# Kernel optimization log

Hardware: AMD Instinct MI355X
Metric: run time of the kernel (lower is better)

The kernel has to match this reference:

```python
import jax, jax.numpy as jnp
import numpy as np

B, N, F_IN, F_OUT, OUT = 32, 1024, 128, 128, 1


def setup_inputs() -> dict:
    key = jax.random.key(0)
    k = jax.random.split(key, 6)
    A = jax.random.uniform(k[0], (B, N, N), dtype=jnp.float32)
    H = jax.random.normal(k[1], (B, N, F_IN), dtype=jnp.float32)
    W = jax.random.normal(k[2], (F_IN, F_OUT), dtype=jnp.float32)
    b = jax.random.normal(k[3], (F_OUT,), dtype=jnp.float32)
    fc_w = jax.random.normal(k[4], (OUT, F_OUT), dtype=jnp.float32)
    fc_b = jax.random.normal(k[5], (OUT,), dtype=jnp.float32)
    return {"A": A, "H": H, "W": W, "b": b, "fc_w": fc_w, "fc_b": fc_b}


def reference(A, H, W, b, fc_w, fc_b):
    n = A.shape[1]
    A_tilde = A + jnp.eye(n, dtype=A.dtype)          # [B,N,N] add self-loops
    d = jnp.sum(A_tilde, axis=1)                      # [B,N] degrees (col sums, matches torch dim=1)
    inv_sqrt_d = 1.0 / jnp.sqrt(d)                    # elementwise, equivalent to sqrt(inv(diag(d)))
    # D^-1/2 A_tilde D^-1/2 as row/col scaling (avoids diag_embed + matrix inverse)
    A_norm = inv_sqrt_d[:, :, None] * A_tilde * inv_sqrt_d[:, None, :]
    h = jax.nn.relu(jnp.einsum('bij,bjf,fo->bio', A_norm, H, W) + b)  # GCN layer
    pooled = jnp.sum(h, axis=1)                       # [B,F_OUT] sum pooling over nodes
    return pooled @ fc_w.T + fc_b                     # [B,OUT]
```

## Files before the change

### kernel.cpp

```cpp
#include <hip/hip_runtime.h>
#include <hip/hip_bf16.h>

#define NB 32
#define NN 1024
#define FF 128

typedef __attribute__((ext_vector_type(8))) short short8;
typedef __attribute__((ext_vector_type(4))) float f32x4;

static __device__ __forceinline__ unsigned short f2bf(float x) {
  unsigned int u = __float_as_uint(x);
  u += 0x7fffu + ((u >> 16) & 1u);
  return (unsigned short)(u >> 16);
}

static __device__ __forceinline__ unsigned long long pack4bf(float a, float b, float c, float d) {
  return (unsigned long long)f2bf(a)
       | ((unsigned long long)f2bf(b) << 16)
       | ((unsigned long long)f2bf(c) << 32)
       | ((unsigned long long)f2bf(d) << 48);
}

static __device__ __forceinline__ void gl16(const void* g, void* l) {
  __builtin_amdgcn_global_load_lds((const __attribute__((address_space(1))) void*)g,
                                   (__attribute__((address_space(3))) void*)l, 16, 0, 0);
}

__global__ __launch_bounds__(256) void k1_colsum_cvt(const float* __restrict__ A,
                                                     unsigned short* __restrict__ Ab,
                                                     float* __restrict__ partial) {
  int t = threadIdx.x;
  int s = blockIdx.x;
  int b = blockIdx.y;
  const float* base = A + (size_t)b * NN * NN + (size_t)(s * 64) * NN + (t << 2);
  unsigned short* obase = Ab + (size_t)b * NN * NN + (size_t)(s * 64) * NN + (t << 2);
  int jj = t << 2;
  bool diag_band = ((t >> 4) == s);
  float4 sum = make_float4(0.f, 0.f, 0.f, 0.f);
  #pragma unroll 8
  for (int i = 0; i < 64; ++i) {
    float4 v = *reinterpret_cast<const float4*>(base + (size_t)i * NN);
    if (diag_band) {
      int gi = (s << 6) + i;
      v.x += (gi == jj)     ? 1.f : 0.f;
      v.y += (gi == jj + 1) ? 1.f : 0.f;
      v.z += (gi == jj + 2) ? 1.f : 0.f;
      v.w += (gi == jj + 3) ? 1.f : 0.f;
    }
    sum.x += v.x; sum.y += v.y; sum.z += v.z; sum.w += v.w;
    *reinterpret_cast<unsigned long long*>(obase + (size_t)i * NN) =
        pack4bf(v.x, v.y, v.z, v.w);
  }
  *reinterpret_cast<float4*>(partial + (((b << 4) + s) << 10) + jj) = sum;
}

__global__ void k2_finalize(const float* __restrict__ partial, const float* __restrict__ W,
                            float* __restrict__ isd, float* __restrict__ pooled,
                            unsigned short* __restrict__ Wt) {
  int idx = blockIdx.x * 256 + threadIdx.x;
  int b = idx >> 10, j = idx & 1023;
  float d = 0.0f;
  #pragma unroll
  for (int s = 0; s < 16; ++s) d += partial[(((b << 4) + s) << 10) + j];
  isd[idx] = rsqrtf(d);
  if (idx < 4096) pooled[idx] = 0.f;
  if (idx < 16384) {
    int o = idx >> 7, k = idx & 127;
    Wt[idx] = f2bf(W[k * FF + o]);
  }
}

__global__ __launch_bounds__(512) void k3_hw(const float* __restrict__ H,
                                             const unsigned short* __restrict__ Wt,
                                             const float* __restrict__ isd,
                                             unsigned short* __restrict__ HWpT) {
  __shared__ unsigned short Ws[128][136];
  __shared__ unsigned short Hs[128][136];
  int jblk = blockIdx.x;
  int b = blockIdx.y;
  int tid = threadIdx.x, wave = tid >> 6, lane = tid & 63;

  {
    int r = tid >> 4, c = (tid & 15) << 3;
    #pragma unroll
    for (int p = 0; p < 4; ++p) {
      int row = r + (p << 5);
      *reinterpret_cast<short8*>(&Ws[row][c]) =
          *reinterpret_cast<const short8*>(Wt + row * FF + c);
    }
  }
  {
    int r = tid >> 5, c = (tid & 31) << 2;
    const float* Hbase = H + (size_t)b * NN * FF + (size_t)(jblk * 128) * FF;
    #pragma unroll
    for (int p = 0; p < 8; ++p) {
      int row = r + (p << 4);
      const float4 v = *reinterpret_cast<const float4*>(Hbase + (size_t)row * FF + c);
      *reinterpret_cast<unsigned long long*>(&Hs[row][c]) = pack4bf(v.x, v.y, v.z, v.w);
    }
  }
  __syncthreads();

  f32x4 acc[8];
  #pragma unroll
  for (int i = 0; i < 8; ++i) acc[i] = (f32x4){0.f, 0.f, 0.f, 0.f};

  int mrow = (wave << 4) + (lane & 15);
  int koff = (lane >> 4) << 3;
  #pragma unroll
  for (int kk = 0; kk < 4; ++kk) {
    short8 af = *reinterpret_cast<const short8*>(&Ws[mrow][(kk << 5) + koff]);
    #pragma unroll
    for (int nf = 0; nf < 8; ++nf) {
      short8 bf = *reinterpret_cast<const short8*>(&Hs[(nf << 4) + (lane & 15)][(kk << 5) + koff]);
      acc[nf] = __builtin_amdgcn_mfma_f32_16x16x32_bf16(af, bf, acc[nf], 0, 0, 0);
    }
  }

  int fbase = (wave << 4) + ((lane >> 4) << 2);
  #pragma unroll
  for (int nf = 0; nf < 8; ++nf) {
    int j = (jblk << 7) + (nf << 4) + (lane & 15);
    float sc = isd[(b << 10) + j];
    size_t outb = (size_t)b * FF * NN + (size_t)j;
    #pragma unroll
    for (int r = 0; r < 4; ++r) {
      HWpT[outb + (size_t)(fbase + r) * NN] = f2bf(acc[nf][r] * sc);
    }
  }
}

__global__ __launch_bounds__(256) void k4_gcn(const unsigned short* __restrict__ Ab,
                                              const unsigned short* __restrict__ HWpT,
                                              const float* __restrict__ isd,
                                              const float* __restrict__ bias,
                                              float* __restrict__ pooled) {
  __shared__ unsigned short As[64 * 64];
  __shared__ unsigned short Bs[128 * 64];
  int iblk = blockIdx.x;
  int b = blockIdx.y;
  int tid = threadIdx.x, wave = tid >> 6, lane = tid & 63;
  int i0 = iblk * 64;

  f32x4 acc[8];
  #pragma unroll
  for (int i = 0; i < 8; ++i) acc[i] = (f32x4){0.f, 0.f, 0.f, 0.f};

  int schunk = (lane & 7) ^ (lane >> 3);
  int arow = (wave << 4) + (lane >> 3);
  int brow = (wave << 5) + (lane >> 3);
  const unsigned short* aSrc = Ab + (size_t)b * NN * NN + (size_t)(i0 + arow) * NN + (schunk << 3);
  const unsigned short* bSrc = HWpT + (size_t)b * FF * NN + (size_t)brow * NN + (schunk << 3);
  char* asBase = (char*)As + wave * 2048;
  char* bsBase = (char*)Bs + wave * 4096;

  int mrow = (wave << 4) + (lane & 15);
  int q16 = (lane >> 4) << 4;
  int aoff0 = (mrow * 128 + q16) ^ ((mrow & 7) << 4);

  for (int k0 = 0; k0 < NN; k0 += 64) {
    gl16(aSrc,               asBase);
    gl16(aSrc + 8 * NN,      asBase + 1024);
    gl16(bSrc,               bsBase);
    gl16(bSrc + 8 * NN,      bsBase + 1024);
    gl16(bSrc + 16 * NN,     bsBase + 2048);
    gl16(bSrc + 24 * NN,     bsBase + 3072);
    __syncthreads();
    #pragma unroll
    for (int kk = 0; kk < 2; ++kk) {
      const short8 af = *reinterpret_cast<const short8*>((const char*)As + (aoff0 ^ (kk << 6)));
      #pragma unroll
      for (int nf = 0; nf < 8; ++nf) {
        int br = (nf << 4) + (lane & 15);
        const short8 bf = *reinterpret_cast<const short8*>(
            (const char*)Bs + ((br * 128 + kk * 64 + q16) ^ ((br & 7) << 4)));
        acc[nf] = __builtin_amdgcn_mfma_f32_16x16x32_bf16(af, bf, acc[nf], 0, 0, 0);
      }
    }
    __syncthreads();
    aSrc += 64; bSrc += 64;
  }

  int irow = i0 + (wave << 4) + ((lane >> 4) << 2);
  float sc0 = isd[(b << 10) + irow];
  float sc1 = isd[(b << 10) + irow + 1];
  float sc2 = isd[(b << 10) + irow + 2];
  float sc3 = isd[(b << 10) + irow + 3];
  #pragma unroll
  for (int nf = 0; nf < 8; ++nf) {
    float bi = bias[(nf << 4) + (lane & 15)];
    float s = fmaxf(acc[nf][0] * sc0 + bi, 0.f)
            + fmaxf(acc[nf][1] * sc1 + bi, 0.f)
            + fmaxf(acc[nf][2] * sc2 + bi, 0.f)
            + fmaxf(acc[nf][3] * sc3 + bi, 0.f);
    s += __shfl_xor(s, 16);
    s += __shfl_xor(s, 32);
    if (lane < 16) atomicAdd(&pooled[(b << 7) + (nf << 4) + lane], s);
  }
}

__global__ void k5_out(const float* __restrict__ pooled, const float* __restrict__ fcw,
                       const float* __restrict__ fcb, float* __restrict__ out) {
  int b = blockIdx.x, t = threadIdx.x;
  float s = pooled[(b << 7) + t] * fcw[t] + pooled[(b << 7) + 64 + t] * fcw[64 + t];
  #pragma unroll
  for (int off = 1; off < 64; off <<= 1) s += __shfl_xor(s, off);
  if (t == 0) out[b] = s + fcb[0];
}

extern "C" void kernel_launch(void* const* d_in, const int* in_sizes, int n_in,
                              void* d_out, int out_size, void* d_ws, size_t ws_size,
                              hipStream_t stream) {
  const float* A    = (const float*)d_in[0];
  const float* H    = (const float*)d_in[1];
  const float* W    = (const float*)d_in[2];
  const float* bias = (const float*)d_in[3];
  const float* fcw  = (const float*)d_in[4];
  const float* fcb  = (const float*)d_in[5];
  float* out = (float*)d_out;

  float* ws = (float*)d_ws;
  float* partial = ws;
  float* isd     = ws + 524288;
  float* pooled  = ws + 524288 + 32768;
  unsigned short* Wt   = (unsigned short*)(ws + 524288 + 32768 + 4096);
  unsigned short* HWpT = Wt + 16384;
  unsigned short* Ab   = HWpT + (size_t)NB * FF * NN;

  k1_colsum_cvt<<<dim3(16, 32), 256, 0, stream>>>(A, Ab, partial);
  k2_finalize  <<<128, 256, 0, stream>>>(partial, W, isd, pooled, Wt);
  k3_hw        <<<dim3(8, 32), 512, 0, stream>>>(H, Wt, isd, HWpT);
  k4_gcn       <<<dim3(16, 32), 256, 0, stream>>>(Ab, HWpT, isd, bias, pooled);
  k5_out       <<<32, 64, 0, stream>>>(pooled, fcw, fcb, out);
}
```

Baseline: 72.59 us.

## Pipeline GCN GEMM with triple-buffered A, register-prefetched B, and staged HW stores

The aggregation GEMM now uses 128-row tiles with a 2x2 wave layout. A is triple-buffered in LDS through async global-to-LDS loads, and B fragments are prefetched directly into registers, so each k-step overlaps loads with MFMA work. Synchronisation uses explicit vmcnt waits plus raw barriers in place of syncthreads, and blocks are remapped so blocks sharing a batch are spread across the grid. Separately, the HW kernel now transposes its output through LDS so global stores are coalesced 16-byte writes. The grid shrinks to 256 blocks and register pressure rises, which risks lower occupancy.

```diff
diff --git a/kernel.cpp b/kernel.cpp
--- a/kernel.cpp
+++ b/kernel.cpp
@@ -117,15 +117,25 @@
     }
   }
 
-  int fbase = (wave << 4) + ((lane >> 4) << 2);
+  int q = lane >> 4, l15 = lane & 15;
   #pragma unroll
   for (int nf = 0; nf < 8; ++nf) {
-    int j = (jblk << 7) + (nf << 4) + (lane & 15);
-    float sc = isd[(b << 10) + j];
-    size_t outb = (size_t)b * FF * NN + (size_t)j;
+    int jl = (nf << 4) + l15;
+    float sc = isd[(b << 10) + (jblk << 7) + jl];
     #pragma unroll
     for (int r = 0; r < 4; ++r) {
-      HWpT[outb + (size_t)(fbase + r) * NN] = f2bf(acc[nf][r] * sc);
+      Ws[(wave << 4) + (q << 2) + r][jl] = f2bf(acc[nf][r] * sc);
+    }
+  }
+  __syncthreads();
+  {
+    unsigned short* obase = HWpT + (size_t)b * FF * NN + (size_t)(jblk * 128);
+    int c8 = (tid & 15) << 3;
+    #pragma unroll
+    for (int p = 0; p < 4; ++p) {
+      int o = (p << 5) + (tid >> 4);
+      *reinterpret_cast<short8*>(obase + (size_t)o * NN + c8) =
+          *reinterpret_cast<const short8*>(&Ws[o][c8]);
     }
   }
 }
@@ -135,67 +145,103 @@
                                               const float* __restrict__ isd,
                                               const float* __restrict__ bias,
                                               float* __restrict__ pooled) {
-  __shared__ unsigned short As[64 * 64];
-  __shared__ unsigned short Bs[128 * 64];
-  int iblk = blockIdx.x;
-  int b = blockIdx.y;
+  __shared__ __align__(1024) char ldsA[3 * 16384];
+  int fid = blockIdx.x;
+  int nid = (fid & 7) * 32 + (fid >> 3);
+  int b = nid >> 3, iblk = nid & 7;
+  int i0 = iblk << 7;
   int tid = threadIdx.x, wave = tid >> 6, lane = tid & 63;
-  int i0 = iblk * 64;
-
-  f32x4 acc[8];
-  #pragma unroll
-  for (int i = 0; i < 8; ++i) acc[i] = (f32x4){0.f, 0.f, 0.f, 0.f};
-
-  int schunk = (lane & 7) ^ (lane >> 3);
-  int arow = (wave << 4) + (lane >> 3);
-  int brow = (wave << 5) + (lane >> 3);
-  const unsigned short* aSrc = Ab + (size_t)b * NN * NN + (size_t)(i0 + arow) * NN + (schunk << 3);
-  const unsigned short* bSrc = HWpT + (size_t)b * FF * NN + (size_t)brow * NN + (schunk << 3);
-  char* asBase = (char*)As + wave * 2048;
-  char* bsBase = (char*)Bs + wave * 4096;
-
-  int mrow = (wave << 4) + (lane & 15);
-  int q16 = (lane >> 4) << 4;
-  int aoff0 = (mrow * 128 + q16) ^ ((mrow & 7) << 4);
-
-  for (int k0 = 0; k0 < NN; k0 += 64) {
-    gl16(aSrc,               asBase);
-    gl16(aSrc + 8 * NN,      asBase + 1024);
-    gl16(bSrc,               bsBase);
-    gl16(bSrc + 8 * NN,      bsBase + 1024);
-    gl16(bSrc + 16 * NN,     bsBase + 2048);
-    gl16(bSrc + 24 * NN,     bsBase + 3072);
-    __syncthreads();
+  int wm = wave >> 1, wn = wave & 1;
+  int l15 = lane & 15, q = lane >> 4;
+  int q16 = q << 4;
+
+  int r8 = lane >> 3;
+  int ch = (lane & 7) ^ r8;
+  const unsigned short* aS = Ab + (size_t)b * NN * NN
+                           + (size_t)(i0 + (wave << 5) + r8) * NN + (ch << 3);
+  char* aD0 = ldsA + (wave << 12);
+
+  const unsigned short* bS = HWpT + (size_t)b * FF * NN
+                           + (size_t)((wn << 6) + l15) * NN + (q << 3);
+
+  f32x4 acc[4][4];
+  #pragma unroll
+  for (int m = 0; m < 4; ++m)
+    #pragma unroll
+    for (int n = 0; n < 4; ++n) acc[m][n] = (f32x4){0.f, 0.f, 0.f, 0.f};
+
+  int swzR = (l15 & 7) << 4;
+  int offA[4];
+  #pragma unroll
+  for (int mr = 0; mr < 4; ++mr)
+    offA[mr] = ((wm << 6) + (mr << 4) + l15) * 128 + q16;
+
+  short8 breg[2][4][2];
+
+#define STAGE_A(buf, k0) { \
+    const unsigned short* s_ = aS + (k0); \
+    char* d_ = ldsA + (buf) * 16384 + (wave << 12); \
+    gl16(s_,           d_); \
+    gl16(s_ + 8 * NN,  d_ + 1024); \
+    gl16(s_ + 16 * NN, d_ + 2048); \
+    gl16(s_ + 24 * NN, d_ + 3072); }
+
+#define LOAD_B(slot, k0) { \
+    _Pragma("unroll") \
+    for (int nf_ = 0; nf_ < 4; ++nf_) { \
+      _Pragma("unroll") \
+      for (int kk_ = 0; kk_ < 2; ++kk_) \
+        breg[slot][nf_][kk_] = *reinterpret_cast<const short8*>( \
+            bS + (size_t)(nf_ << 4) * NN + (k0) + (kk_ << 5)); } }
+
+  STAGE_A(0, 0)
+  STAGE_A(1, 64)
+  LOAD_B(0, 0)
+
+  #pragma unroll
+  for (int t = 0; t < 16; ++t) {
+    if (t < 15) LOAD_B((t + 1) & 1, (t + 1) * 64)
+    if (t < 14) STAGE_A((t + 2) % 3, (t + 2) * 64)
+    if (t < 14)      asm volatile("s_waitcnt vmcnt(16)" ::: "memory");
+    else if (t == 14) asm volatile("s_waitcnt vmcnt(12)" ::: "memory");
+    else              asm volatile("s_waitcnt vmcnt(0)" ::: "memory");
+    __builtin_amdgcn_s_barrier();
+    const char* Abuf = ldsA + (t % 3) * 16384;
     #pragma unroll
     for (int kk = 0; kk < 2; ++kk) {
-      const short8 af = *reinterpret_cast<const short8*>((const char*)As + (aoff0 ^ (kk << 6)));
+      short8 af[4];
       #pragma unroll
-      for (int nf = 0; nf < 8; ++nf) {
-        int br = (nf << 4) + (lane & 15);
-        const short8 bf = *reinterpret_cast<const short8*>(
-            (const char*)Bs + ((br * 128 + kk * 64 + q16) ^ ((br & 7) << 4)));
-        acc[nf] = __builtin_amdgcn_mfma_f32_16x16x32_bf16(af, bf, acc[nf], 0, 0, 0);
-      }
-    }
-    __syncthreads();
-    aSrc += 64; bSrc += 64;
-  }
-
-  int irow = i0 + (wave << 4) + ((lane >> 4) << 2);
-  float sc0 = isd[(b << 10) + irow];
-  float sc1 = isd[(b << 10) + irow + 1];
-  float sc2 = isd[(b << 10) + irow + 2];
-  float sc3 = isd[(b << 10) + irow + 3];
-  #pragma unroll
-  for (int nf = 0; nf < 8; ++nf) {
-    float bi = bias[(nf << 4) + (lane & 15)];
-    float s = fmaxf(acc[nf][0] * sc0 + bi, 0.f)
-            + fmaxf(acc[nf][1] * sc1 + bi, 0.f)
-            + fmaxf(acc[nf][2] * sc2 + bi, 0.f)
-            + fmaxf(acc[nf][3] * sc3 + bi, 0.f);
-    s += __shfl_xor(s, 16);
-    s += __shfl_xor(s, 32);
-    if (lane < 16) atomicAdd(&pooled[(b << 7) + (nf << 4) + lane], s);
+      for (int mr = 0; mr < 4; ++mr)
+        af[mr] = *reinterpret_cast<const short8*>(Abuf + ((offA[mr] + (kk << 6)) ^ swzR));
+      #pragma unroll
+      for (int mr = 0; mr < 4; ++mr)
+        #pragma unroll
+        for (int nf = 0; nf < 4; ++nf)
+          acc[mr][nf] = __builtin_amdgcn_mfma_f32_16x16x32_bf16(
+              af[mr], breg[t & 1][nf][kk], acc[mr][nf], 0, 0, 0);
+    }
+    __builtin_amdgcn_s_barrier();
+  }
+#undef STAGE_A
+#undef LOAD_B
+
+  #pragma unroll
+  for (int nf = 0; nf < 4; ++nf) {
+    int f = (wn << 6) + (nf << 4) + l15;
+    float bi = bias[f];
+    float stot = 0.f;
+    #pragma unroll
+    for (int mr = 0; mr < 4; ++mr) {
+      int irow = i0 + (wm << 6) + (mr << 4) + (q << 2);
+      const f32x4 sc = *reinterpret_cast<const f32x4*>(isd + (b << 10) + irow);
+      stot += fmaxf(acc[mr][nf][0] * sc[0] + bi, 0.f)
+            + fmaxf(acc[mr][nf][1] * sc[1] + bi, 0.f)
+            + fmaxf(acc[mr][nf][2] * sc[2] + bi, 0.f)
+            + fmaxf(acc[mr][nf][3] * sc[3] + bi, 0.f);
+    }
+    stot += __shfl_xor(stot, 16);
+    stot += __shfl_xor(stot, 32);
+    if (lane < 16) atomicAdd(&pooled[(b << 7) + f], stot);
   }
 }
 
@@ -230,6 +276,6 @@
   k1_colsum_cvt<<<dim3(16, 32), 256, 0, stream>>>(A, Ab, partial);
   k2_finalize  <<<128, 256, 0, stream>>>(partial, W, isd, pooled, Wt);
   k3_hw        <<<dim3(8, 32), 512, 0, stream>>>(H, Wt, isd, HWpT);
-  k4_gcn       <<<dim3(16, 32), 256, 0, stream>>>(Ab, HWpT, isd, bias, pooled);
+  k4_gcn       <<<256, 256, 0, stream>>>(Ab, HWpT, isd, bias, pooled);
   k5_out       <<<32, 64, 0, stream>>>(pooled, fcw, fcb, out);
 }
```

Measured after the change: 73.20 us. About the same (+0.8%).
